# Kernel tuning notes

Hardware: AMD Instinct MI355X
Metric: run time of the kernel (lower is better)

Reference implementation:

```python
import jax, jax.numpy as jnp
import numpy as np

T = 512          # tokens
H = 2048         # hidden_size
E = 256          # n_routed_experts (8 groups x 32)
G = 8            # tucker groups
EPG = 32         # experts per group
K = 6            # top_k
I = 1408         # moe_intermediate_size
R1 = 128         # tucker input rank
R2 = 128         # tucker output rank


def setup_inputs() -> dict:
    key = jax.random.key(0)
    ks = jax.random.split(key, 12)
    s = 0.02
    return {
        "hidden_states": jax.random.normal(ks[0], (T, H), jnp.float32),
        "w_router": jax.random.normal(ks[1], (H, E), jnp.float32) * s,
        # gate_proj Tucker factors: H -> I
        "U_in_gate": jax.random.normal(ks[2], (G, H, R1), jnp.float32) * s,
        "core_gate": jax.random.normal(ks[3], (E, R1, R2), jnp.float32) * s,
        "U_out_gate": jax.random.normal(ks[4], (G, I, R2), jnp.float32) * s,
        # up_proj Tucker factors: H -> I
        "U_in_up": jax.random.normal(ks[5], (G, H, R1), jnp.float32) * s,
        "core_up": jax.random.normal(ks[6], (E, R1, R2), jnp.float32) * s,
        "U_out_up": jax.random.normal(ks[7], (G, I, R2), jnp.float32) * s,
        # down_proj Tucker factors: I -> H
        "U_in_down": jax.random.normal(ks[8], (G, I, R1), jnp.float32) * s,
        "core_down": jax.random.normal(ks[9], (E, R1, R2), jnp.float32) * s,
        "U_out_down": jax.random.normal(ks[10], (G, H, R2), jnp.float32) * s,
    }


def _tucker_apply(x, g, e, U_in, core, U_out):
    """Per-expert Tucker linear: y_t = ((x_t @ U_in[g_t]) @ core[e_t]) @ U_out[g_t].T
    x: [Td, din]; g: [Td] group ids; e: [Td] full expert ids.
    U_in: [G, din, r1]; core: [E, r1, r2]; U_out: [G, dout, r2]."""
    h1 = jnp.einsum('td,gdr->tgr', x, U_in)                       # [Td, G, r1]
    h1 = jnp.take_along_axis(h1, g[:, None, None], axis=1)[:, 0]  # [Td, r1]
    h2 = jnp.einsum('tr,trs->ts', h1, core[e])                    # [Td, r2]
    y = jnp.einsum('ts,gds->tgd', h2, U_out)                      # [Td, G, dout]
    return jnp.take_along_axis(y, g[:, None, None], axis=1)[:, 0]


def reference(hidden_states, w_router, U_in_gate, core_gate, U_out_gate,
              U_in_up, core_up, U_out_up, U_in_down, core_down, U_out_down):
    n_tok, hid = hidden_states.shape
    router_logits = hidden_states @ w_router                          # [T, E]
    probs = jax.nn.softmax(router_logits.astype(jnp.float32), axis=-1)
    routing_weights, selected = jax.lax.top_k(probs, K)               # [T, K]
    routing_weights = routing_weights / routing_weights.sum(-1, keepdims=True)
    routing_weights = routing_weights.astype(hidden_states.dtype)

    xd = jnp.repeat(hidden_states, K, axis=0)                         # [T*K, H]
    e = selected.reshape(-1)                                          # [T*K]
    g = e // EPG                                                      # group ids

    gate_out = _tucker_apply(xd, g, e, U_in_gate, core_gate, U_out_gate)
    up_out = _tucker_apply(xd, g, e, U_in_up, core_up, U_out_up)
    inter = jax.nn.silu(gate_out) * up_out                            # [T*K, I]
    down_out = _tucker_apply(inter, g, e, U_in_down, core_down, U_out_down)

    combined = (down_out.reshape(n_tok, K, hid) * routing_weights[..., None]).sum(axis=1)
    return combined
```

## Files before the change

### kernel.cpp

```cpp
#include <hip/hip_runtime.h>
#include <cmath>
#include <cstdint>

#define TNUM 512
#define HID 2048
#define NEXP 256
#define NGRP 8
#define KTOP 6
#define IDIM 1408
#define RNK 128
#define NPAIR (TNUM*KTOP)
#define NRCAP 3328
#define MAXTILES (NRCAP/32)

typedef _Float16 f16;
typedef f16  f16x8 __attribute__((ext_vector_type(8)));
typedef f16  f16x4 __attribute__((ext_vector_type(4)));
typedef float f32x4 __attribute__((ext_vector_type(4)));
#define MFMA16(a,b,c) __builtin_amdgcn_mfma_f32_16x16x32_f16((a),(b),(c),0,0,0)

static __device__ __forceinline__ float4 ld4(const float* p){ return *reinterpret_cast<const float4*>(p); }
static __device__ __forceinline__ void st4(float* p, float4 v){ *reinterpret_cast<float4*>(p) = v; }
static __device__ __forceinline__ f16x8 ldh8(const f16* p){ return *reinterpret_cast<const f16x8*>(p); }

constexpr size_t A256(size_t x){ return (x + 255) & ~(size_t)255; }
constexpr size_t OFF_SEL    = 0;
constexpr size_t OFF_WT     = A256(OFF_SEL    + (size_t)NPAIR*4);
constexpr size_t OFF_CNT    = A256(OFF_WT     + (size_t)NPAIR*4);
constexpr size_t OFF_ESTART = A256(OFF_CNT    + (size_t)NEXP*4);
constexpr size_t OFF_TG     = A256(OFF_ESTART + (size_t)NEXP*4);
constexpr size_t OFF_HDR    = A256(OFF_TG     + (size_t)MAXTILES*4);
constexpr size_t OFF_ROWT   = A256(OFF_HDR    + 16);
constexpr size_t OFF_ROWW   = A256(OFF_ROWT   + (size_t)NRCAP*4);
constexpr size_t OFF_BIG    = A256(OFF_ROWW   + (size_t)NRCAP*4);

constexpr size_t SZ_XH    = (size_t)TNUM*HID*2;
constexpr size_t SZ_UTI   = (size_t)NGRP*RNK*HID*2;
constexpr size_t SZ_CT    = (size_t)NEXP*RNK*RNK*2;
constexpr size_t SZ_H1ALL = (size_t)2*TNUM*NGRP*RNK*2;
constexpr size_t SZ_UO    = (size_t)NGRP*IDIM*RNK*2;
constexpr size_t SZ_UOD   = (size_t)NGRP*HID*RNK*2;
constexpr size_t SZ_WR    = (size_t)NEXP*HID*2;
constexpr size_t SZ_H2    = (size_t)NRCAP*RNK*2;
constexpr size_t SZ_INTER = (size_t)NRCAP*IDIM*2;

constexpr size_t OFF_XH    = OFF_BIG;
constexpr size_t OFF_XL    = OFF_XH   + SZ_XH;
constexpr size_t OFF_UTIG  = OFF_XL   + SZ_XH;
constexpr size_t OFF_UTIU  = OFF_UTIG + SZ_UTI;
constexpr size_t OFF_CGT   = OFF_UTIU + SZ_UTI;
constexpr size_t OFF_CUT   = OFF_CGT  + SZ_CT;
constexpr size_t OFF_H1    = OFF_CUT  + SZ_CT;
constexpr size_t REG_END   = OFF_H1   + SZ_H1ALL;
constexpr size_t OFF_INTER = OFF_XH;
constexpr size_t OFF_LPART = OFF_H1;
constexpr size_t OFF_UOG   = REG_END;
constexpr size_t OFF_UOU   = OFF_UOG  + SZ_UO;
constexpr size_t OFF_UTID  = OFF_UOU  + SZ_UO;
constexpr size_t OFF_UOD   = OFF_UTID + SZ_UO;
constexpr size_t OFF_CDT   = OFF_UOD  + SZ_UOD;
constexpr size_t OFF_WRH   = OFF_CDT  + SZ_CT;
constexpr size_t OFF_WRL   = OFF_WRH  + SZ_WR;
constexpr size_t OFF_H2G   = OFF_WRL  + SZ_WR;
constexpr size_t OFF_H2U   = OFF_H2G  + SZ_H2;
constexpr size_t OFF_D1    = OFF_H2U  + SZ_H2;
constexpr size_t OFF_D2    = OFF_D1   + SZ_H2;
constexpr size_t WS_NEED   = OFF_D2   + SZ_H2;
static_assert(OFF_INTER + SZ_INTER <= OFF_CGT, "inter overlay must end before cores");
static_assert(SZ_H1ALL >= (size_t)4*TNUM*NEXP*4/2 || true, "");

__global__ __launch_bounds__(256) void k_cvt_all(
    const float* __restrict__ x,   const float* __restrict__ Uog,
    const float* __restrict__ Uou, const float* __restrict__ Uod,
    f16* __restrict__ xh, f16* __restrict__ xl,
    f16* __restrict__ uog, f16* __restrict__ uou, f16* __restrict__ uod){
  const int b = blockIdx.x, tid = threadIdx.x;
  if(b < 1024){
    const size_t i = (size_t)b*256 + tid;
    float4 v = ld4(x + i*4);
    f16x4 H, L;
    H[0]=(f16)v.x; L[0]=(f16)(v.x-(float)H[0]);
    H[1]=(f16)v.y; L[1]=(f16)(v.y-(float)H[1]);
    H[2]=(f16)v.z; L[2]=(f16)(v.z-(float)H[2]);
    H[3]=(f16)v.w; L[3]=(f16)(v.w-(float)H[3]);
    *reinterpret_cast<f16x4*>(xh + i*4) = H;
    *reinterpret_cast<f16x4*>(xl + i*4) = L;
    return;
  }
  const float* in; f16* hi; size_t i;
  if(b < 2432){        in = Uog; hi = uog; i = (size_t)(b-1024)*256 + tid; }
  else if(b < 3840){   in = Uou; hi = uou; i = (size_t)(b-2432)*256 + tid; }
  else {               in = Uod; hi = uod; i = (size_t)(b-3840)*256 + tid; }
  float4 v = ld4(in + i*4);
  f16x4 H;
  H[0]=(f16)(v.x*16.f); H[1]=(f16)(v.y*16.f); H[2]=(f16)(v.z*16.f); H[3]=(f16)(v.w*16.f);
  *reinterpret_cast<f16x4*>(hi + i*4) = H;
}

__global__ __launch_bounds__(256) void k_cvt_wr(const float* __restrict__ w,
                                                f16* __restrict__ wh, f16* __restrict__ wl){
  __shared__ float tile[32][33];
  const int r0 = blockIdx.y*32, c0 = blockIdx.x*32;
  const int tid = threadIdx.x;
  { const int r = tid>>3, c4 = (tid&7)*4;
    float4 v = ld4(w + (size_t)(r0+r)*NEXP + c0 + c4);
    tile[r][c4]=v.x; tile[r][c4+1]=v.y; tile[r][c4+2]=v.z; tile[r][c4+3]=v.w; }
  __syncthreads();
  { const int c = tid>>3, r4 = (tid&7)*4;
    f16x4 H, L;
    #pragma unroll
    for(int k = 0; k < 4; k++){
      float v = tile[r4+k][c]*16.f;
      H[k] = (f16)v; L[k] = (f16)(v - (float)H[k]);
    }
    const size_t o = (size_t)(c0+c)*HID + r0 + r4;
    *reinterpret_cast<f16x4*>(wh + o) = H;
    *reinterpret_cast<f16x4*>(wl + o) = L; }
}

__global__ __launch_bounds__(256) void k_cvt_t3(
    const float* __restrict__ Uig, const float* __restrict__ Uiu, const float* __restrict__ Uid,
    f16* __restrict__ ig, f16* __restrict__ iu, f16* __restrict__ idn){
  __shared__ float tile[32][33];
  const int z = blockIdx.z, tensor = z>>3, g = z&7;
  const float* in; f16* hi; int R;
  if(tensor == 0){ in = Uig; hi = ig; R = HID; }
  else if(tensor == 1){ in = Uiu; hi = iu; R = HID; }
  else { in = Uid; hi = idn; R = IDIM; }
  const int r0 = blockIdx.y*32, c0 = blockIdx.x*32;
  if(r0 >= R) return;
  const int tid = threadIdx.x;
  { const int r = tid>>3, c4 = (tid&7)*4;
    float4 v = ld4(in + ((size_t)g*R + r0 + r)*RNK + c0 + c4);
    tile[r][c4]=v.x; tile[r][c4+1]=v.y; tile[r][c4+2]=v.z; tile[r][c4+3]=v.w; }
  __syncthreads();
  { const int c = tid>>3, r4 = (tid&7)*4;
    f16x4 H;
    #pragma unroll
    for(int k = 0; k < 4; k++) H[k] = (f16)(tile[r4+k][c]*16.f);
    *reinterpret_cast<f16x4*>(hi + ((size_t)g*RNK + c0 + c)*R + r0 + r4) = H; }
}

__global__ __launch_bounds__(256) void k_cvt_core(
    const float* __restrict__ cg, const float* __restrict__ cu, const float* __restrict__ cd,
    f16* __restrict__ cgt, f16* __restrict__ cut, f16* __restrict__ cdt){
  __shared__ float tile[32][33];
  const int z = blockIdx.z, tensor = z>>8, e = z&255;
  const float* in; f16* o;
  if(tensor == 0){ in = cg; o = cgt; }
  else if(tensor == 1){ in = cu; o = cut; }
  else { in = cd; o = cdt; }
  in += (size_t)e*RNK*RNK; o += (size_t)e*RNK*RNK;
  const int r0 = blockIdx.y*32, c0 = blockIdx.x*32;
  const int tid = threadIdx.x;
  { const int r = tid>>3, c4 = (tid&7)*4;
    float4 v = ld4(in + (size_t)(r0+r)*RNK + c0 + c4);
    tile[r][c4]=v.x; tile[r][c4+1]=v.y; tile[r][c4+2]=v.z; tile[r][c4+3]=v.w; }
  __syncthreads();
  { const int c = tid>>3, r4 = (tid&7)*4;
    f16x4 H;
    #pragma unroll
    for(int k = 0; k < 4; k++) H[k] = (f16)(tile[r4+k][c]*16.f);
    *reinterpret_cast<f16x4*>(o + (size_t)(c0+c)*RNK + r0 + r4) = H; }
}

__global__ __launch_bounds__(256) void k_router_mfma(
    const f16* __restrict__ xh, const f16* __restrict__ xl,
    const f16* __restrict__ wh, const f16* __restrict__ wl,
    float* __restrict__ lpart){
  __shared__ float red[4][32][64];
  const int m = blockIdx.x, ecol = blockIdx.y, kz = blockIdx.z;
  const int tid = threadIdx.x;
  const int wid = tid>>6, lane = tid&63, q = lane>>4, id = lane&15;
  const int r0 = m*32, e0 = ecol*64;
  const int kb = kz*512 + wid*128;
  f32x4 acc[2][4];
  #pragma unroll
  for(int f = 0; f < 2; f++)
    #pragma unroll
    for(int c = 0; c < 4; c++) acc[f][c] = (f32x4){0.f,0.f,0.f,0.f};
  #pragma unroll
  for(int kk = 0; kk < 128; kk += 32){
    const size_t a0 = (size_t)(r0+id)*HID    + kb + kk + q*8;
    const size_t a1 = (size_t)(r0+16+id)*HID + kb + kk + q*8;
    f16x8 ah0 = ldh8(xh + a0), al0 = ldh8(xl + a0);
    f16x8 ah1 = ldh8(xh + a1), al1 = ldh8(xl + a1);
    #pragma unroll
    for(int c = 0; c < 4; c++){
      const size_t bo = (size_t)(e0 + c*16 + id)*HID + kb + kk + q*8;
      f16x8 bh = ldh8(wh + bo);
      f16x8 bl = ldh8(wl + bo);
      acc[0][c] = MFMA16(ah0, bh, acc[0][c]);
      acc[0][c] = MFMA16(ah0, bl, acc[0][c]);
      acc[0][c] = MFMA16(al0, bh, acc[0][c]);
      acc[1][c] = MFMA16(ah1, bh, acc[1][c]);
      acc[1][c] = MFMA16(ah1, bl, acc[1][c]);
      acc[1][c] = MFMA16(al1, bh, acc[1][c]);
    }
  }
  #pragma unroll
  for(int f = 0; f < 2; f++)
    #pragma unroll
    for(int c = 0; c < 4; c++)
      #pragma unroll
      for(int r = 0; r < 4; r++)
        red[wid][f*16 + q*4 + r][c*16 + id] = acc[f][c][r];
  __syncthreads();
  const int row = tid>>3, c8 = (tid&7)*8;
  float o[8];
  #pragma unroll
  for(int j = 0; j < 8; j++)
    o[j] = (red[0][row][c8+j] + red[1][row][c8+j] + red[2][row][c8+j] + red[3][row][c8+j])*0.0625f;
  float* dst = &lpart[((size_t)kz*TNUM + r0 + row)*NEXP + e0 + c8];
  st4(dst,     make_float4(o[0],o[1],o[2],o[3]));
  st4(dst + 4, make_float4(o[4],o[5],o[6],o[7]));
}

__global__ __launch_bounds__(256) void k_topk(const float* __restrict__ lpart,
                                              int* __restrict__ sel,
                                              float* __restrict__ wt,
                                              int* __restrict__ cnt){
  __shared__ float wv[4];
  __shared__ int   wi[4];
  __shared__ float swin[KTOP];
  __shared__ int   iwin[KTOP];
  const int t = blockIdx.x, tid = threadIdx.x;
  const int lane = tid & 63, wid = tid >> 6;
  const size_t base = (size_t)t*NEXP + tid;
  float v = lpart[base] + lpart[base + (size_t)TNUM*NEXP]
          + lpart[base + (size_t)2*TNUM*NEXP] + lpart[base + (size_t)3*TNUM*NEXP];
  for(int k = 0; k < KTOP; k++){
    float cv = v; int ci = tid;
    #pragma unroll
    for(int off = 1; off < 64; off <<= 1){
      float ov = __shfl_xor(cv, off);
      int   oi = __shfl_xor(ci, off);
      if(ov > cv || (ov == cv && oi < ci)){ cv = ov; ci = oi; }
    }
    if(lane == 0){ wv[wid] = cv; wi[wid] = ci; }
    __syncthreads();
    if(tid == 0){
      float bv = wv[0]; int bi = wi[0];
      #pragma unroll
      for(int w2 = 1; w2 < 4; w2++)
        if(wv[w2] > bv || (wv[w2] == bv && wi[w2] < bi)){ bv = wv[w2]; bi = wi[w2]; }
      swin[k] = bv; iwin[k] = bi;
    }
    __syncthreads();
    if(tid == iwin[k]) v = -INFINITY;
  }
  if(tid == 0){
    float mx = swin[0], s = 0.f, ww[KTOP];
    #pragma unroll
    for(int k = 0; k < KTOP; k++){ ww[k] = expf(swin[k]-mx); s += ww[k]; }
    float inv = 1.f/s;
    #pragma unroll
    for(int k = 0; k < KTOP; k++){
      sel[t*KTOP+k] = iwin[k];
      wt[t*KTOP+k]  = ww[k]*inv;
      atomicAdd(&cnt[iwin[k]], 1);
    }
  }
}

__global__ __launch_bounds__(256) void k_meta_scatter(
    const int* __restrict__ cnt, const int* __restrict__ sel, const float* __restrict__ wt,
    int* __restrict__ estart, int* __restrict__ tile_group, int* __restrict__ hdr,
    int* __restrict__ row_t, float* __restrict__ row_w){
  __shared__ int scnt[256];
  __shared__ int gsum[8];
  __shared__ int g0[9];
  __shared__ int curs[256];
  const int tid = threadIdx.x;
  scnt[tid] = cnt[tid];
  if(tid < 8) gsum[tid] = 0;
  __syncthreads();
  atomicAdd(&gsum[tid>>5], scnt[tid]);
  __syncthreads();
  if(tid == 0){
    int run = 0;
    for(int g = 0; g < 8; g++){ g0[g] = run; run += (gsum[g]+31) & ~31; }
    g0[8] = run; hdr[0] = run>>5; hdr[1] = run;
  }
  __syncthreads();
  int g = tid >> 5, s = g0[g];
  for(int i = (g<<5); i < tid; i++) s += scnt[i];
  estart[tid] = s; curs[tid] = s;
  const int nt = g0[8] >> 5;
  for(int t2 = tid; t2 < MAXTILES; t2 += 256){
    int gg = -1;
    if(t2 < nt){
      for(int g2 = 0; g2 < 8; g2++) if(t2*32 >= g0[g2] && t2*32 < g0[g2+1]) gg = g2;
    }
    tile_group[t2] = gg;
  }
  for(int i = tid; i < NRCAP; i += 256) row_w[i] = 0.f;
  __syncthreads();
  for(int p = tid; p < NPAIR; p += 256){
    const int e = sel[p];
    const int pos = atomicAdd(&curs[e], 1);
    row_t[pos] = p / KTOP;
    row_w[pos] = wt[p];
  }
}

__global__ __launch_bounds__(256) void k_mm_stage1(
    const f16* __restrict__ xh,
    const f16* __restrict__ Bg_, const f16* __restrict__ Bu_,
    f16* __restrict__ H1){
  __shared__ float red[4][32][64];
  const int m = blockIdx.x, nt = blockIdx.y;
  const int pu = nt>>4, g = (nt>>1)&7, ch = nt&1;
  const f16* B = (pu ? Bu_ : Bg_) + (size_t)g*RNK*HID + (size_t)ch*64*HID;
  const int tid = threadIdx.x;
  const int wid = tid>>6, lane = tid&63, q = lane>>4, id = lane&15;
  const int kb = wid*512;
  const int r0 = m*32;
  f32x4 acc[2][4];
  #pragma unroll
  for(int f = 0; f < 2; f++)
    #pragma unroll
    for(int c = 0; c < 4; c++) acc[f][c] = (f32x4){0.f,0.f,0.f,0.f};
  #pragma unroll 4
  for(int kk = 0; kk < 512; kk += 32){
    f16x8 a0 = ldh8(xh + (size_t)(r0+id)*HID    + kb + kk + q*8);
    f16x8 a1 = ldh8(xh + (size_t)(r0+16+id)*HID + kb + kk + q*8);
    #pragma unroll
    for(int c = 0; c < 4; c++){
      f16x8 b = ldh8(B + (size_t)(c*16+id)*HID + kb + kk + q*8);
      acc[0][c] = MFMA16(a0, b, acc[0][c]);
      acc[1][c] = MFMA16(a1, b, acc[1][c]);
    }
  }
  #pragma unroll
  for(int f = 0; f < 2; f++)
    #pragma unroll
    for(int c = 0; c < 4; c++)
      #pragma unroll
      for(int r = 0; r < 4; r++)
        red[wid][f*16 + q*4 + r][c*16 + id] = acc[f][c][r];
  __syncthreads();
  f16* out = H1 + (size_t)pu*TNUM*(NGRP*RNK);
  const int row = tid>>3, c8 = (tid&7)*8;
  f16x8 o8;
  #pragma unroll
  for(int j = 0; j < 8; j++)
    o8[j] = (f16)(red[0][row][c8+j] + red[1][row][c8+j] + red[2][row][c8+j] + red[3][row][c8+j]);
  *reinterpret_cast<f16x8*>(&out[(size_t)(r0+row)*(NGRP*RNK) + g*RNK + ch*64 + c8]) = o8;
}

__global__ __launch_bounds__(256) void k_core2(
    const f16* __restrict__ Cg, const f16* __restrict__ Cu,
    const f16* __restrict__ H1,
    const int* __restrict__ estart, const int* __restrict__ cnt,
    const int* __restrict__ row_t,
    f16* __restrict__ h2g, f16* __restrict__ h2u){
  const int e = blockIdx.x, up = blockIdx.y;
  const int n = cnt[e];
  if(n == 0) return;
  const int j0 = estart[e], g = e >> 5;
  const f16* C = (up ? Cu : Cg) + (size_t)e*RNK*RNK;
  const f16* A = H1 + (size_t)up*TNUM*(NGRP*RNK);
  f16* o = up ? h2u : h2g;
  const int tid = threadIdx.x;
  const int wid = tid>>6, lane = tid&63, q = lane>>4, id = lane&15;
  for(int rt = 0; rt*16 < n; rt++){
    const int jrow = j0 + rt*16 + id;
    const int jj = jrow < j0+n ? jrow : j0;
    const f16* arow = A + (size_t)row_t[jj]*(NGRP*RNK) + g*RNK;
    f32x4 acc0 = (f32x4){0.f,0.f,0.f,0.f};
    f32x4 acc1 = (f32x4){0.f,0.f,0.f,0.f};
    #pragma unroll
    for(int kk = 0; kk < RNK; kk += 32){
      f16x8 a = ldh8(arow + kk + q*8);
      f16x8 b0 = ldh8(C + (size_t)(wid*32 + id)*RNK      + kk + q*8);
      f16x8 b1 = ldh8(C + (size_t)(wid*32 + 16 + id)*RNK + kk + q*8);
      acc0 = MFMA16(a, b0, acc0);
      acc1 = MFMA16(a, b1, acc1);
    }
    #pragma unroll
    for(int r = 0; r < 4; r++){
      const int j = j0 + rt*16 + q*4 + r;
      if(j < j0+n){
        o[(size_t)j*RNK + wid*32 + id]      = (f16)acc0[r];
        o[(size_t)j*RNK + wid*32 + 16 + id] = (f16)acc1[r];
      }
    }
  }
}

__global__ __launch_bounds__(128) void k_mm_gateup(
    const f16* __restrict__ Ag, const f16* __restrict__ Au,
    const f16* __restrict__ Bg, const f16* __restrict__ Bu,
    const int* __restrict__ tg,
    f16* __restrict__ inter){
  const int g = tg[blockIdx.x];
  if(g < 0) return;
  const int j0 = blockIdx.x*32;
  const int tid = threadIdx.x;
  const int wid = tid>>6, lane = tid&63, q = lane>>4, id = lane&15;
  const int c0 = blockIdx.y*128 + wid*64;
  const size_t bbase = (size_t)g*IDIM*RNK;
  f32x4 accg[2][4], accu[2][4];
  #pragma unroll
  for(int f = 0; f < 2; f++)
    #pragma unroll
    for(int c = 0; c < 4; c++){ accg[f][c] = (f32x4){0.f,0.f,0.f,0.f}; accu[f][c] = (f32x4){0.f,0.f,0.f,0.f}; }
  #pragma unroll 2
  for(int kk = 0; kk < RNK; kk += 32){
    const size_t a0off = (size_t)(j0+id)*RNK    + kk + q*8;
    const size_t a1off = (size_t)(j0+16+id)*RNK + kk + q*8;
    f16x8 ag0 = ldh8(Ag + a0off), ag1 = ldh8(Ag + a1off);
    f16x8 au0 = ldh8(Au + a0off), au1 = ldh8(Au + a1off);
    #pragma unroll
    for(int c = 0; c < 4; c++){
      const size_t boff = bbase + (size_t)(c0 + c*16 + id)*RNK + kk + q*8;
      f16x8 bg = ldh8(Bg + boff);
      f16x8 bu = ldh8(Bu + boff);
      accg[0][c] = MFMA16(ag0, bg, accg[0][c]);
      accg[1][c] = MFMA16(ag1, bg, accg[1][c]);
      accu[0][c] = MFMA16(au0, bu, accu[0][c]);
      accu[1][c] = MFMA16(au1, bu, accu[1][c]);
    }
  }
  #pragma unroll
  for(int f = 0; f < 2; f++)
    #pragma unroll
    for(int c = 0; c < 4; c++)
      #pragma unroll
      for(int r = 0; r < 4; r++){
        float vg = accg[f][c][r] * (1.f/4096.f);
        float vu = accu[f][c][r] * (1.f/4096.f);
        float sv = vg/(1.f+expf(-vg))*vu*256.f;
        inter[(size_t)(j0 + f*16 + q*4 + r)*IDIM + c0 + c*16 + id] = (f16)sv;
      }
}

__global__ __launch_bounds__(256) void k_mm_down_in(
    const f16* __restrict__ A_, const f16* __restrict__ B_,
    const int* __restrict__ tg,
    f16* __restrict__ d1){
  __shared__ float red[4][32][64];
  const int g = tg[blockIdx.x];
  if(g < 0) return;
  const int j0 = blockIdx.x*32;
  const int ch = blockIdx.y;
  const f16* B = B_ + (size_t)g*RNK*IDIM + (size_t)ch*64*IDIM;
  const int tid = threadIdx.x;
  const int wid = tid>>6, lane = tid&63, q = lane>>4, id = lane&15;
  const int kb = wid*352;
  f32x4 acc[2][4];
  #pragma unroll
  for(int f = 0; f < 2; f++)
    #pragma unroll
    for(int c = 0; c < 4; c++) acc[f][c] = (f32x4){0.f,0.f,0.f,0.f};
  #pragma unroll 2
  for(int kk = 0; kk < 352; kk += 32){
    f16x8 a0 = ldh8(A_ + (size_t)(j0+id)*IDIM    + kb + kk + q*8);
    f16x8 a1 = ldh8(A_ + (size_t)(j0+16+id)*IDIM + kb + kk + q*8);
    #pragma unroll
    for(int c = 0; c < 4; c++){
      f16x8 b = ldh8(B + (size_t)(c*16+id)*IDIM + kb + kk + q*8);
      acc[0][c] = MFMA16(a0, b, acc[0][c]);
      acc[1][c] = MFMA16(a1, b, acc[1][c]);
    }
  }
  #pragma unroll
  for(int f = 0; f < 2; f++)
    #pragma unroll
    for(int c = 0; c < 4; c++)
      #pragma unroll
      for(int r = 0; r < 4; r++)
        red[wid][f*16 + q*4 + r][c*16 + id] = acc[f][c][r];
  __syncthreads();
  const int row = tid>>3, c8 = (tid&7)*8;
  f16x8 o8;
  #pragma unroll
  for(int j = 0; j < 8; j++)
    o8[j] = (f16)(red[0][row][c8+j] + red[1][row][c8+j] + red[2][row][c8+j] + red[3][row][c8+j]);
  *reinterpret_cast<f16x8*>(&d1[(size_t)(j0+row)*RNK + ch*64 + c8]) = o8;
}

__global__ __launch_bounds__(256) void k_core_down(
    const f16* __restrict__ Cd,
    const f16* __restrict__ d1,
    const int* __restrict__ estart, const int* __restrict__ cnt,
    f16* __restrict__ d2){
  const int e = blockIdx.x;
  const int n = cnt[e];
  if(n == 0) return;
  const int j0 = estart[e];
  const f16* C = Cd + (size_t)e*RNK*RNK;
  const int tid = threadIdx.x;
  const int wid = tid>>6, lane = tid&63, q = lane>>4, id = lane&15;
  for(int rt = 0; rt*16 < n; rt++){
    const int jrow = j0 + rt*16 + id;
    const int jj = jrow < j0+n ? jrow : j0;
    const f16* arow = d1 + (size_t)jj*RNK;
    f32x4 acc0 = (f32x4){0.f,0.f,0.f,0.f};
    f32x4 acc1 = (f32x4){0.f,0.f,0.f,0.f};
    #pragma unroll
    for(int kk = 0; kk < RNK; kk += 32){
      f16x8 a = ldh8(arow + kk + q*8);
      f16x8 b0 = ldh8(C + (size_t)(wid*32 + id)*RNK      + kk + q*8);
      f16x8 b1 = ldh8(C + (size_t)(wid*32 + 16 + id)*RNK + kk + q*8);
      acc0 = MFMA16(a, b0, acc0);
      acc1 = MFMA16(a, b1, acc1);
    }
    #pragma unroll
    for(int r = 0; r < 4; r++){
      const int j = j0 + rt*16 + q*4 + r;
      if(j < j0+n){
        d2[(size_t)j*RNK + wid*32 + id]      = (f16)acc0[r];
        d2[(size_t)j*RNK + wid*32 + 16 + id] = (f16)acc1[r];
      }
    }
  }
}

__global__ __launch_bounds__(128) void k_mm_down_out(
    const f16* __restrict__ A_, const f16* __restrict__ B_,
    const int* __restrict__ tg,
    const int* __restrict__ row_t, const float* __restrict__ row_w,
    float* __restrict__ out){
  const int g = tg[blockIdx.x];
  if(g < 0) return;
  const int j0 = blockIdx.x*32;
  const f16* B = B_ + (size_t)g*HID*RNK;
  const int tid = threadIdx.x;
  const int wid = tid>>6, lane = tid&63, q = lane>>4, id = lane&15;
  const int c0 = blockIdx.y*128 + wid*64;
  f32x4 acc[2][4];
  #pragma unroll
  for(int f = 0; f < 2; f++)
    #pragma unroll
    for(int c = 0; c < 4; c++) acc[f][c] = (f32x4){0.f,0.f,0.f,0.f};
  #pragma unroll 2
  for(int kk = 0; kk < RNK; kk += 32){
    f16x8 a0 = ldh8(A_ + (size_t)(j0+id)*RNK    + kk + q*8);
    f16x8 a1 = ldh8(A_ + (size_t)(j0+16+id)*RNK + kk + q*8);
    #pragma unroll
    for(int c = 0; c < 4; c++){
      f16x8 b = ldh8(B + (size_t)(c0 + c*16 + id)*RNK + kk + q*8);
      acc[0][c] = MFMA16(a0, b, acc[0][c]);
      acc[1][c] = MFMA16(a1, b, acc[1][c]);
    }
  }
  #pragma unroll
  for(int f = 0; f < 2; f++)
    #pragma unroll
    for(int r = 0; r < 4; r++){
      const int j = j0 + f*16 + q*4 + r;
      const float w = row_w[j];
      if(w != 0.f){
        const size_t obase = (size_t)row_t[j]*HID;
        #pragma unroll
        for(int c = 0; c < 4; c++)
          atomicAdd(&out[obase + c0 + c*16 + id], acc[f][c][r]*w*(1.f/1048576.f));
      }
    }
}

extern "C" void kernel_launch(void* const* d_in, const int* in_sizes, int n_in,
                              void* d_out, int out_size, void* d_ws, size_t ws_size,
                              hipStream_t stream){
  const float* x   = (const float*)d_in[0];
  const float* wr  = (const float*)d_in[1];
  const float* Uig = (const float*)d_in[2];
  const float* cg  = (const float*)d_in[3];
  const float* Uog = (const float*)d_in[4];
  const float* Uiu = (const float*)d_in[5];
  const float* cu  = (const float*)d_in[6];
  const float* Uou = (const float*)d_in[7];
  const float* Uid = (const float*)d_in[8];
  const float* cd  = (const float*)d_in[9];
  const float* Uod = (const float*)d_in[10];
  float* out = (float*)d_out;
  char* ws = (char*)d_ws;
  if(ws_size < WS_NEED) return;

  int*   sel    = (int*)  (ws + OFF_SEL);
  float* wt     = (float*)(ws + OFF_WT);
  int*   cnt    = (int*)  (ws + OFF_CNT);
  int*   estart = (int*)  (ws + OFF_ESTART);
  int*   tg     = (int*)  (ws + OFF_TG);
  int*   hdr    = (int*)  (ws + OFF_HDR);
  int*   row_t  = (int*)  (ws + OFF_ROWT);
  float* row_w  = (float*)(ws + OFF_ROWW);
  float* lpart  = (float*)(ws + OFF_LPART);
  f16* xh    = (f16*)(ws + OFF_XH);
  f16* xl    = (f16*)(ws + OFF_XL);
  f16* utig  = (f16*)(ws + OFF_UTIG);
  f16* utiu  = (f16*)(ws + OFF_UTIU);
  f16* cgt   = (f16*)(ws + OFF_CGT);
  f16* cut   = (f16*)(ws + OFF_CUT);
  f16* cdt   = (f16*)(ws + OFF_CDT);
  f16* H1    = (f16*)(ws + OFF_H1);
  f16* uog   = (f16*)(ws + OFF_UOG);
  f16* uou   = (f16*)(ws + OFF_UOU);
  f16* utid  = (f16*)(ws + OFF_UTID);
  f16* uod   = (f16*)(ws + OFF_UOD);
  f16* wrh   = (f16*)(ws + OFF_WRH);
  f16* wrl   = (f16*)(ws + OFF_WRL);
  f16* h2g   = (f16*)(ws + OFF_H2G);
  f16* h2u   = (f16*)(ws + OFF_H2U);
  f16* inter = (f16*)(ws + OFF_INTER);
  f16* d1    = (f16*)(ws + OFF_D1);
  f16* d2    = (f16*)(ws + OFF_D2);

  hipMemsetAsync(cnt, 0, NEXP*sizeof(int), stream);
  hipMemsetAsync(out, 0, (size_t)TNUM*HID*sizeof(float), stream);

  k_cvt_all  <<<5888,              256, 0, stream>>>(x, Uog, Uou, Uod, xh, xl, uog, uou, uod);
  k_cvt_wr   <<<dim3(8,64),        256, 0, stream>>>(wr, wrh, wrl);

  k_router_mfma<<<dim3(16,4,4),    256, 0, stream>>>(xh, xl, wrh, wrl, lpart);
  k_topk     <<<TNUM,              256, 0, stream>>>(lpart, sel, wt, cnt);
  k_meta_scatter<<<1,              256, 0, stream>>>(cnt, sel, wt, estart, tg, hdr, row_t, row_w);

  k_cvt_t3   <<<dim3(4,64,24),     256, 0, stream>>>(Uig, Uiu, Uid, utig, utiu, utid);
  k_cvt_core <<<dim3(4,4,768),     256, 0, stream>>>(cg, cu, cd, cgt, cut, cdt);

  k_mm_stage1<<<dim3(16,32),       256, 0, stream>>>(xh, utig, utiu, H1);
  k_core2    <<<dim3(NEXP,2),      256, 0, stream>>>(cgt, cut, H1, estart, cnt, row_t, h2g, h2u);
  k_mm_gateup<<<dim3(MAXTILES,11), 128, 0, stream>>>(h2g, h2u, uog, uou, tg, inter);
  k_mm_down_in<<<dim3(MAXTILES,2), 256, 0, stream>>>(inter, utid, tg, d1);
  k_core_down<<<NEXP,              256, 0, stream>>>(cdt, d1, estart, cnt, d2);
  k_mm_down_out<<<dim3(MAXTILES,16),128,0, stream>>>(d2, uod, tg, row_t, row_w, out);
}
```

Measured before the change: 168.9 us.

## Replace atomic scatter-add with per-row down output plus deterministic combine kernel

The down-projection output kernel now writes each sorted row's result to a dense fp32 buffer, and a new combine kernel gathers the K rows per token via a pair-to-position map and applies routing weights. This removes the fp32 atomicAdd scatter into the output and the full output memset. The weight-conversion launches are also merged into two kernels, and the expert-count reset is folded into the first one, which cuts launch count and memsets. The cost is an extra round trip through a ~27MB intermediate buffer and one more launch.

```diff
diff --git a/kernel.cpp b/kernel.cpp
--- a/kernel.cpp
+++ b/kernel.cpp
@@ -31,8 +31,8 @@
 constexpr size_t OFF_TG     = A256(OFF_ESTART + (size_t)NEXP*4);
 constexpr size_t OFF_HDR    = A256(OFF_TG     + (size_t)MAXTILES*4);
 constexpr size_t OFF_ROWT   = A256(OFF_HDR    + 16);
-constexpr size_t OFF_ROWW   = A256(OFF_ROWT   + (size_t)NRCAP*4);
-constexpr size_t OFF_BIG    = A256(OFF_ROWW   + (size_t)NRCAP*4);
+constexpr size_t OFF_POS    = A256(OFF_ROWT   + (size_t)NRCAP*4);
+constexpr size_t OFF_BIG    = A256(OFF_POS    + (size_t)NPAIR*4);
 
 constexpr size_t SZ_XH    = (size_t)TNUM*HID*2;
 constexpr size_t SZ_UTI   = (size_t)NGRP*RNK*HID*2;
@@ -43,6 +43,7 @@
 constexpr size_t SZ_WR    = (size_t)NEXP*HID*2;
 constexpr size_t SZ_H2    = (size_t)NRCAP*RNK*2;
 constexpr size_t SZ_INTER = (size_t)NRCAP*IDIM*2;
+constexpr size_t SZ_DOWNO = (size_t)NRCAP*HID*4;
 
 constexpr size_t OFF_XH    = OFF_BIG;
 constexpr size_t OFF_XL    = OFF_XH   + SZ_XH;
@@ -53,6 +54,7 @@
 constexpr size_t OFF_H1    = OFF_CUT  + SZ_CT;
 constexpr size_t REG_END   = OFF_H1   + SZ_H1ALL;
 constexpr size_t OFF_INTER = OFF_XH;
+constexpr size_t OFF_DOWNO = OFF_XH;
 constexpr size_t OFF_LPART = OFF_H1;
 constexpr size_t OFF_UOG   = REG_END;
 constexpr size_t OFF_UOU   = OFF_UOG  + SZ_UO;
@@ -67,13 +69,17 @@
 constexpr size_t OFF_D2    = OFF_D1   + SZ_H2;
 constexpr size_t WS_NEED   = OFF_D2   + SZ_H2;
 static_assert(OFF_INTER + SZ_INTER <= OFF_CGT, "inter overlay must end before cores");
-static_assert(SZ_H1ALL >= (size_t)4*TNUM*NEXP*4/2 || true, "");
-
-__global__ __launch_bounds__(256) void k_cvt_all(
+static_assert(OFF_DOWNO + SZ_DOWNO <= OFF_UOG, "downo overlay must end before persistent tail");
+
+__global__ __launch_bounds__(256) void k_cvt_main(
     const float* __restrict__ x,   const float* __restrict__ Uog,
     const float* __restrict__ Uou, const float* __restrict__ Uod,
+    const float* __restrict__ wr,
     f16* __restrict__ xh, f16* __restrict__ xl,
-    f16* __restrict__ uog, f16* __restrict__ uou, f16* __restrict__ uod){
+    f16* __restrict__ uog, f16* __restrict__ uou, f16* __restrict__ uod,
+    f16* __restrict__ wh, f16* __restrict__ wl,
+    int* __restrict__ cnt){
+  __shared__ float tile[32][33];
   const int b = blockIdx.x, tid = threadIdx.x;
   if(b < 1024){
     const size_t i = (size_t)b*256 + tid;
@@ -87,23 +93,22 @@
     *reinterpret_cast<f16x4*>(xl + i*4) = L;
     return;
   }
-  const float* in; f16* hi; size_t i;
-  if(b < 2432){        in = Uog; hi = uog; i = (size_t)(b-1024)*256 + tid; }
-  else if(b < 3840){   in = Uou; hi = uou; i = (size_t)(b-2432)*256 + tid; }
-  else {               in = Uod; hi = uod; i = (size_t)(b-3840)*256 + tid; }
-  float4 v = ld4(in + i*4);
-  f16x4 H;
-  H[0]=(f16)(v.x*16.f); H[1]=(f16)(v.y*16.f); H[2]=(f16)(v.z*16.f); H[3]=(f16)(v.w*16.f);
-  *reinterpret_cast<f16x4*>(hi + i*4) = H;
-}
-
-__global__ __launch_bounds__(256) void k_cvt_wr(const float* __restrict__ w,
-                                                f16* __restrict__ wh, f16* __restrict__ wl){
-  __shared__ float tile[32][33];
-  const int r0 = blockIdx.y*32, c0 = blockIdx.x*32;
-  const int tid = threadIdx.x;
+  if(b < 5888){
+    const float* in; f16* hi; size_t i;
+    if(b < 2432){        in = Uog; hi = uog; i = (size_t)(b-1024)*256 + tid; }
+    else if(b < 3840){   in = Uou; hi = uou; i = (size_t)(b-2432)*256 + tid; }
+    else {               in = Uod; hi = uod; i = (size_t)(b-3840)*256 + tid; }
+    float4 v = ld4(in + i*4);
+    f16x4 H;
+    H[0]=(f16)(v.x*16.f); H[1]=(f16)(v.y*16.f); H[2]=(f16)(v.z*16.f); H[3]=(f16)(v.w*16.f);
+    *reinterpret_cast<f16x4*>(hi + i*4) = H;
+    return;
+  }
+  const int wb = b - 5888;
+  if(wb == 0) cnt[tid] = 0;
+  const int c0 = (wb & 7)*32, r0 = (wb >> 3)*32;
   { const int r = tid>>3, c4 = (tid&7)*4;
-    float4 v = ld4(w + (size_t)(r0+r)*NEXP + c0 + c4);
+    float4 v = ld4(wr + (size_t)(r0+r)*NEXP + c0 + c4);
     tile[r][c4]=v.x; tile[r][c4+1]=v.y; tile[r][c4+2]=v.z; tile[r][c4+3]=v.w; }
   __syncthreads();
   { const int c = tid>>3, r4 = (tid&7)*4;
@@ -118,41 +123,33 @@
     *reinterpret_cast<f16x4*>(wl + o) = L; }
 }
 
-__global__ __launch_bounds__(256) void k_cvt_t3(
+__global__ __launch_bounds__(256) void k_cvt_t(
     const float* __restrict__ Uig, const float* __restrict__ Uiu, const float* __restrict__ Uid,
-    f16* __restrict__ ig, f16* __restrict__ iu, f16* __restrict__ idn){
-  __shared__ float tile[32][33];
-  const int z = blockIdx.z, tensor = z>>3, g = z&7;
-  const float* in; f16* hi; int R;
-  if(tensor == 0){ in = Uig; hi = ig; R = HID; }
-  else if(tensor == 1){ in = Uiu; hi = iu; R = HID; }
-  else { in = Uid; hi = idn; R = IDIM; }
-  const int r0 = blockIdx.y*32, c0 = blockIdx.x*32;
-  if(r0 >= R) return;
-  const int tid = threadIdx.x;
-  { const int r = tid>>3, c4 = (tid&7)*4;
-    float4 v = ld4(in + ((size_t)g*R + r0 + r)*RNK + c0 + c4);
-    tile[r][c4]=v.x; tile[r][c4+1]=v.y; tile[r][c4+2]=v.z; tile[r][c4+3]=v.w; }
-  __syncthreads();
-  { const int c = tid>>3, r4 = (tid&7)*4;
-    f16x4 H;
-    #pragma unroll
-    for(int k = 0; k < 4; k++) H[k] = (f16)(tile[r4+k][c]*16.f);
-    *reinterpret_cast<f16x4*>(hi + ((size_t)g*RNK + c0 + c)*R + r0 + r4) = H; }
-}
-
-__global__ __launch_bounds__(256) void k_cvt_core(
-    const float* __restrict__ cg, const float* __restrict__ cu, const float* __restrict__ cd,
+    const float* __restrict__ cg,  const float* __restrict__ cu,  const float* __restrict__ cd,
+    f16* __restrict__ ig, f16* __restrict__ iu, f16* __restrict__ idn,
     f16* __restrict__ cgt, f16* __restrict__ cut, f16* __restrict__ cdt){
   __shared__ float tile[32][33];
-  const int z = blockIdx.z, tensor = z>>8, e = z&255;
-  const float* in; f16* o;
-  if(tensor == 0){ in = cg; o = cgt; }
-  else if(tensor == 1){ in = cu; o = cut; }
-  else { in = cd; o = cdt; }
-  in += (size_t)e*RNK*RNK; o += (size_t)e*RNK*RNK;
-  const int r0 = blockIdx.y*32, c0 = blockIdx.x*32;
-  const int tid = threadIdx.x;
+  const int b = blockIdx.x, tid = threadIdx.x;
+  const float* in; f16* o; int r0, c0, R, OR;
+  if(b < 6144){
+    const int cx = b & 3, ry = (b>>2) & 63, z = b >> 8;
+    const int tensor = z >> 3, g = z & 7;
+    if(tensor == 0){ in = Uig; o = ig; R = HID; }
+    else if(tensor == 1){ in = Uiu; o = iu; R = HID; }
+    else { in = Uid; o = idn; R = IDIM; }
+    r0 = ry*32; c0 = cx*32;
+    if(r0 >= R) return;
+    in += (size_t)g*R*RNK; o += (size_t)g*RNK*R;
+    OR = R;
+  } else {
+    const int cb = b - 6144;
+    const int tensor = cb >> 12, rem = cb & 4095, e = rem >> 4;
+    if(tensor == 0){ in = cg; o = cgt; }
+    else if(tensor == 1){ in = cu; o = cut; }
+    else { in = cd; o = cdt; }
+    in += (size_t)e*RNK*RNK; o += (size_t)e*RNK*RNK;
+    r0 = ((rem>>2)&3)*32; c0 = (rem&3)*32; R = RNK; OR = RNK;
+  }
   { const int r = tid>>3, c4 = (tid&7)*4;
     float4 v = ld4(in + (size_t)(r0+r)*RNK + c0 + c4);
     tile[r][c4]=v.x; tile[r][c4+1]=v.y; tile[r][c4+2]=v.z; tile[r][c4+3]=v.w; }
@@ -161,7 +158,7 @@
     f16x4 H;
     #pragma unroll
     for(int k = 0; k < 4; k++) H[k] = (f16)(tile[r4+k][c]*16.f);
-    *reinterpret_cast<f16x4*>(o + (size_t)(c0+c)*RNK + r0 + r4) = H; }
+    *reinterpret_cast<f16x4*>(o + (size_t)(c0+c)*OR + r0 + r4) = H; }
 }
 
 __global__ __launch_bounds__(256) void k_router_mfma(
@@ -264,9 +261,9 @@
 }
 
 __global__ __launch_bounds__(256) void k_meta_scatter(
-    const int* __restrict__ cnt, const int* __restrict__ sel, const float* __restrict__ wt,
+    const int* __restrict__ cnt, const int* __restrict__ sel,
     int* __restrict__ estart, int* __restrict__ tile_group, int* __restrict__ hdr,
-    int* __restrict__ row_t, float* __restrict__ row_w){
+    int* __restrict__ row_t, int* __restrict__ pos_of_pair){
   __shared__ int scnt[256];
   __shared__ int gsum[8];
   __shared__ int g0[9];
@@ -294,13 +291,12 @@
     }
     tile_group[t2] = gg;
   }
-  for(int i = tid; i < NRCAP; i += 256) row_w[i] = 0.f;
   __syncthreads();
   for(int p = tid; p < NPAIR; p += 256){
     const int e = sel[p];
     const int pos = atomicAdd(&curs[e], 1);
     row_t[pos] = p / KTOP;
-    row_w[pos] = wt[p];
+    pos_of_pair[p] = pos;
   }
 }
 
@@ -521,8 +517,7 @@
 __global__ __launch_bounds__(128) void k_mm_down_out(
     const f16* __restrict__ A_, const f16* __restrict__ B_,
     const int* __restrict__ tg,
-    const int* __restrict__ row_t, const float* __restrict__ row_w,
-    float* __restrict__ out){
+    float* __restrict__ downo){
   const int g = tg[blockIdx.x];
   if(g < 0) return;
   const int j0 = blockIdx.x*32;
@@ -549,16 +544,29 @@
   #pragma unroll
   for(int f = 0; f < 2; f++)
     #pragma unroll
-    for(int r = 0; r < 4; r++){
-      const int j = j0 + f*16 + q*4 + r;
-      const float w = row_w[j];
-      if(w != 0.f){
-        const size_t obase = (size_t)row_t[j]*HID;
-        #pragma unroll
-        for(int c = 0; c < 4; c++)
-          atomicAdd(&out[obase + c0 + c*16 + id], acc[f][c][r]*w*(1.f/1048576.f));
-      }
-    }
+    for(int c = 0; c < 4; c++)
+      #pragma unroll
+      for(int r = 0; r < 4; r++)
+        downo[(size_t)(j0 + f*16 + q*4 + r)*HID + c0 + c*16 + id] = acc[f][c][r]*(1.f/1048576.f);
+}
+
+__global__ __launch_bounds__(256) void k_combine(const float* __restrict__ downo,
+                                                 const int* __restrict__ pos_of_pair,
+                                                 const float* __restrict__ wt,
+                                                 float* __restrict__ out){
+  const int idx = blockIdx.x*256 + threadIdx.x;
+  const int t  = idx >> 9;
+  const int h4 = (idx & 511) << 2;
+  float4 acc = make_float4(0.f,0.f,0.f,0.f);
+  #pragma unroll
+  for(int k = 0; k < KTOP; k++){
+    const int p = t*KTOP + k;
+    const float w = wt[p];
+    const int pos = pos_of_pair[p];
+    float4 v = ld4(&downo[(size_t)pos*HID + h4]);
+    acc.x += w*v.x; acc.y += w*v.y; acc.z += w*v.z; acc.w += w*v.w;
+  }
+  st4(&out[(size_t)t*HID + h4], acc);
 }
 
 extern "C" void kernel_launch(void* const* d_in, const int* in_sizes, int n_in,
@@ -586,7 +594,7 @@
   int*   tg     = (int*)  (ws + OFF_TG);
   int*   hdr    = (int*)  (ws + OFF_HDR);
   int*   row_t  = (int*)  (ws + OFF_ROWT);
-  float* row_w  = (float*)(ws + OFF_ROWW);
+  int*   pos    = (int*)  (ws + OFF_POS);
   float* lpart  = (float*)(ws + OFF_LPART);
   f16* xh    = (f16*)(ws + OFF_XH);
   f16* xl    = (f16*)(ws + OFF_XL);
@@ -607,24 +615,22 @@
   f16* inter = (f16*)(ws + OFF_INTER);
   f16* d1    = (f16*)(ws + OFF_D1);
   f16* d2    = (f16*)(ws + OFF_D2);
-
-  hipMemsetAsync(cnt, 0, NEXP*sizeof(int), stream);
-  hipMemsetAsync(out, 0, (size_t)TNUM*HID*sizeof(float), stream);
-
-  k_cvt_all  <<<5888,              256, 0, stream>>>(x, Uog, Uou, Uod, xh, xl, uog, uou, uod);
-  k_cvt_wr   <<<dim3(8,64),        256, 0, stream>>>(wr, wrh, wrl);
+  float* downo = (float*)(ws + OFF_DOWNO);
+
+  k_cvt_main <<<6400,              256, 0, stream>>>(x, Uog, Uou, Uod, wr,
+                                                     xh, xl, uog, uou, uod, wrh, wrl, cnt);
+  k_cvt_t    <<<18432,             256, 0, stream>>>(Uig, Uiu, Uid, cg, cu, cd,
+                                                     utig, utiu, utid, cgt, cut, cdt);
 
   k_router_mfma<<<dim3(16,4,4),    256, 0, stream>>>(xh, xl, wrh, wrl, lpart);
   k_topk     <<<TNUM,              256, 0, stream>>>(lpart, sel, wt, cnt);
-  k_meta_scatter<<<1,              256, 0, stream>>>(cnt, sel, wt, estart, tg, hdr, row_t, row_w);
-
-  k_cvt_t3   <<<dim3(4,64,24),     256, 0, stream>>>(Uig, Uiu, Uid, utig, utiu, utid);
-  k_cvt_core <<<dim3(4,4,768),     256, 0, stream>>>(cg, cu, cd, cgt, cut, cdt);
+  k_meta_scatter<<<1,              256, 0, stream>>>(cnt, sel, estart, tg, hdr, row_t, pos);
 
   k_mm_stage1<<<dim3(16,32),       256, 0, stream>>>(xh, utig, utiu, H1);
   k_core2    <<<dim3(NEXP,2),      256, 0, stream>>>(cgt, cut, H1, estart, cnt, row_t, h2g, h2u);
   k_mm_gateup<<<dim3(MAXTILES,11), 128, 0, stream>>>(h2g, h2u, uog, uou, tg, inter);
   k_mm_down_in<<<dim3(MAXTILES,2), 256, 0, stream>>>(inter, utid, tg, d1);
   k_core_down<<<NEXP,              256, 0, stream>>>(cdt, d1, estart, cnt, d2);
-  k_mm_down_out<<<dim3(MAXTILES,16),128,0, stream>>>(d2, uod, tg, row_t, row_w, out);
-}
+  k_mm_down_out<<<dim3(MAXTILES,16),128,0, stream>>>(d2, uod, tg, downo);
+  k_combine  <<<1024,              256, 0, stream>>>(downo, pos, wt, out);
+}
```

Measured after the change: 146.1 us. 13.5% less time.
